# Kernel optimization log

Measured on AMD Instinct MI355X. Metric: run time of the kernel, lower is better.

Reference implementation:

```python
import jax, jax.numpy as jnp
import numpy as np

DIM = 192
HEADS = 4
EPS = 1e-12  # F.normalize default eps


def setup_inputs() -> dict:
    key = jax.random.key(0)
    k0, k1, k2, k3 = jax.random.split(key, 4)
    x = jax.random.normal(k0, (4, DIM, 128, 128), dtype=jnp.float32)
    # qkv 1x1 conv weight: [3*dim, dim, 1, 1] -> stored as [3*dim, dim]
    w_qkv = jax.random.normal(k1, (3 * DIM, DIM), dtype=jnp.float32) * (1.0 / np.sqrt(DIM))
    # depthwise 3x3 conv weight: [3*dim, 1, 3, 3]
    w_dw = jax.random.normal(k2, (3 * DIM, 1, 3, 3), dtype=jnp.float32) * (1.0 / 3.0)
    # project_out 1x1 conv weight: [dim, dim]
    w_proj = jax.random.normal(k3, (DIM, DIM), dtype=jnp.float32) * (1.0 / np.sqrt(DIM))
    # temperature: ones(heads,1,1), requires_grad=False in original
    temperature = jnp.ones((HEADS, 1, 1), dtype=jnp.float32)
    return {"x": x, "w_qkv": w_qkv, "w_dw": w_dw, "w_proj": w_proj,
            "temperature": temperature}


def _l2norm(t):
    # F.normalize(t, dim=-1): t / max(||t||_2, eps)
    n = jnp.sqrt(jnp.sum(t * t, axis=-1, keepdims=True))
    return t / jnp.maximum(n, EPS)


def reference(x, w_qkv, w_dw, w_proj, temperature):
    b, c, h, w = x.shape
    ch = c // HEADS  # channels per head
    # 1x1 conv (no bias) == channel GEMM
    qkv = jnp.einsum('oc,bchw->bohw', w_qkv, x)
    # depthwise 3x3 conv, padding=1, groups=3*dim
    qkv = jax.lax.conv_general_dilated(
        qkv, w_dw, window_strides=(1, 1), padding=((1, 1), (1, 1)),
        dimension_numbers=('NCHW', 'OIHW', 'NCHW'),
        feature_group_count=3 * c)
    q, k, v = jnp.split(qkv, 3, axis=1)
    # b (head ch) h w -> b head ch (h w)
    def rearr(t):
        return t.reshape(b, HEADS, ch, h * w)
    q, k, v = rearr(q), rearr(k), rearr(v)
    q = _l2norm(q)
    k = _l2norm(k)
    # channel-channel attention: [b, head, ch, ch]
    attn = jnp.einsum('bhcn,bhdn->bhcd', q, k) * temperature[None]
    attn = jax.nn.softmax(attn, axis=-1)
    out = jnp.einsum('bhcd,bhdn->bhcn', attn, v)
    out = out.reshape(b, c, h, w)
    out = jnp.einsum('oc,bchw->bohw', w_proj, out)
    return out
```

## Files before the change

### kernel.cpp

```cpp
#include <hip/hip_runtime.h>

typedef unsigned short u16;
typedef float f32x4 __attribute__((ext_vector_type(4)));
typedef __bf16 bf16x8 __attribute__((ext_vector_type(8)));
typedef unsigned short u16x8 __attribute__((ext_vector_type(8)));
typedef unsigned short u16x4 __attribute__((ext_vector_type(4)));

#define DEV static __device__ __forceinline__

DEV u16 f2bf(float f) {
  unsigned int u = __float_as_uint(f);
  u += 0x7FFFu + ((u >> 16) & 1u);
  return (u16)(u >> 16);
}
DEV float bf2f(u16 h) { return __uint_as_float(((unsigned int)h) << 16); }

DEV void gload_lds16(const void* g, void* l) {
  __builtin_amdgcn_global_load_lds(
      (__attribute__((address_space(1))) void*)(unsigned long long)g,
      (__attribute__((address_space(3))) void*)l, 16, 0, 0);
}

__global__ __launch_bounds__(256) void convert_w_kernel(
    const float* __restrict__ in, u16* __restrict__ out, int n) {
  int i = blockIdx.x * 256 + threadIdx.x;
  if (i < n) out[i] = f2bf(in[i]);
}

template <bool IN_F32, bool OUT_BF16, int NJ>
__global__ __launch_bounds__(256, 3) void gemm_bt_kernel(
    const void* __restrict__ Av, const u16* __restrict__ B,
    void* __restrict__ Cv, size_t aBatch, size_t bBatch, size_t cBatch,
    int ldC) {
  __shared__ __align__(16) char smem[49152];
  char* sA = smem;
  char* sB = smem + 24576;

  const int tid = threadIdx.x, wave = tid >> 6, lane = tid & 63;
  const int id = blockIdx.x;
  const int m0 = (id & 255) * 64, b = id >> 8;

  if (IN_F32) {
    const float* Xb = (const float*)Av + (size_t)b * aBatch + m0;
    const int cbl = tid & 15, iq = tid >> 4;
#pragma unroll
    for (int pass = 0; pass < 3; ++pass) {
      const int cb = pass * 16 + cbl;
      f32x4 v[4];
#pragma unroll
      for (int r = 0; r < 4; ++r)
        v[r] = *(const f32x4*)(Xb + (size_t)(cb * 4 + r) * 16384 + iq * 4);
#pragma unroll
      for (int j = 0; j < 4; ++j) {
        const int n = iq * 4 + j;
        u16x4 col;
        col[0] = f2bf(v[0][j]);
        col[1] = f2bf(v[1][j]);
        col[2] = f2bf(v[2][j]);
        col[3] = f2bf(v[3][j]);
        *(u16x4*)(sA + n * 384 + ((cb * 8) ^ ((n & 7) << 4))) = col;
      }
    }
  } else {
    const u16* Vb = (const u16*)Av + (size_t)b * aBatch + m0;
#pragma unroll
    for (int pass = 0; pass < 2; ++pass) {
      const int task = pass * 256 + tid;
      if (task < 384) {
        const int cb = task >> 3, io = task & 7;
        u16x8 v[4];
#pragma unroll
        for (int r = 0; r < 4; ++r)
          v[r] = *(const u16x8*)(Vb + (size_t)(cb * 4 + r) * 16384 + io * 8);
#pragma unroll
        for (int j = 0; j < 8; ++j) {
          const int n = io * 8 + j;
          u16x4 col;
          col[0] = v[0][j];
          col[1] = v[1][j];
          col[2] = v[2][j];
          col[3] = v[3][j];
          *(u16x4*)(sA + n * 384 + ((cb * 8) ^ ((n & 7) << 4))) = col;
        }
      }
    }
  }
  const char* Bbase = (const char*)(B + (size_t)b * bBatch);
#pragma unroll
  for (int i = 0; i < 6; ++i) {
    const int c = i * 4 + wave;
    const int d = c * 1024 + lane * 16;
    const int row = d / 384, inrow = d - row * 384;
    gload_lds16(Bbase + row * 384 + (inrow ^ ((row & 7) << 4)), sB + c * 1024);
  }
  asm volatile("s_waitcnt vmcnt(0) lgkmcnt(0)" ::: "memory");
  __builtin_amdgcn_s_barrier();

  const int wm = wave & 1, wn = wave >> 1;
  const int l15 = lane & 15, lg = lane >> 4;
  const int swm = (l15 & 7) << 4;
  const int rA0 = (wm * 32 + l15) * 384;
  const int rB0 = (wn * 32 + l15) * 384;

  bf16x8 af[2][6];
#pragma unroll
  for (int mi = 0; mi < 2; ++mi)
#pragma unroll
    for (int ks = 0; ks < 6; ++ks)
      af[mi][ks] = *(const bf16x8*)(sA + rA0 + mi * 16 * 384 +
                                    ((ks * 64 + lg * 16) ^ swm));

  f32x4 acc[2][2];
#pragma unroll 1
  for (int j = 0; j < NJ; ++j) {
    bf16x8 bfv[2][6];
#pragma unroll
    for (int nj = 0; nj < 2; ++nj)
#pragma unroll
      for (int ks = 0; ks < 6; ++ks)
        bfv[nj][ks] = *(const bf16x8*)(sB + rB0 + nj * 16 * 384 +
                                       ((ks * 64 + lg * 16) ^ swm));
    asm volatile("s_waitcnt lgkmcnt(0)" ::: "memory");
    __builtin_amdgcn_s_barrier();
    if (j + 1 < NJ) {
      const char* Bj = Bbase + (size_t)(j + 1) * 24576;
#pragma unroll
      for (int i = 0; i < 6; ++i) {
        const int c = i * 4 + wave;
        const int d = c * 1024 + lane * 16;
        const int row = d / 384, inrow = d - row * 384;
        gload_lds16(Bj + row * 384 + (inrow ^ ((row & 7) << 4)), sB + c * 1024);
      }
    }
    if (j > 0) {
      const int j0 = (j - 1) * 64;
      if (OUT_BF16) {
        u16* Cb = (u16*)Cv + (size_t)b * cBatch;
#pragma unroll
        for (int mi = 0; mi < 2; ++mi)
#pragma unroll
          for (int nj = 0; nj < 2; ++nj) {
            u16x4 ov;
#pragma unroll
            for (int r = 0; r < 4; ++r) ov[r] = f2bf(acc[mi][nj][r]);
            *(u16x4*)(Cb + (size_t)(j0 + wn * 32 + nj * 16 + l15) * ldC + m0 +
                      wm * 32 + mi * 16 + lg * 4) = ov;
          }
      } else {
        float* Cb = (float*)Cv + (size_t)b * cBatch;
#pragma unroll
        for (int mi = 0; mi < 2; ++mi)
#pragma unroll
          for (int nj = 0; nj < 2; ++nj)
            *(f32x4*)(Cb + (size_t)(j0 + wn * 32 + nj * 16 + l15) * ldC + m0 +
                      wm * 32 + mi * 16 + lg * 4) = acc[mi][nj];
      }
    }
    __builtin_amdgcn_sched_barrier(0);
#pragma unroll
    for (int mi = 0; mi < 2; ++mi)
#pragma unroll
      for (int nj = 0; nj < 2; ++nj) acc[mi][nj] = (f32x4){0.f, 0.f, 0.f, 0.f};
#pragma unroll
    for (int ks = 0; ks < 6; ++ks)
#pragma unroll
      for (int mi = 0; mi < 2; ++mi)
#pragma unroll
        for (int nj = 0; nj < 2; ++nj)
          acc[mi][nj] = __builtin_amdgcn_mfma_f32_16x16x32_bf16(
              af[mi][ks], bfv[nj][ks], acc[mi][nj], 0, 0, 0);
    if (j + 1 < NJ) {
      if (j == 0)
        asm volatile("s_waitcnt vmcnt(0)" ::: "memory");
      else
        asm volatile("s_waitcnt vmcnt(4)" ::: "memory");
      __builtin_amdgcn_s_barrier();
    }
  }
  {
    const int j0 = (NJ - 1) * 64;
    if (OUT_BF16) {
      u16* Cb = (u16*)Cv + (size_t)b * cBatch;
#pragma unroll
      for (int mi = 0; mi < 2; ++mi)
#pragma unroll
        for (int nj = 0; nj < 2; ++nj) {
          u16x4 ov;
#pragma unroll
          for (int r = 0; r < 4; ++r) ov[r] = f2bf(acc[mi][nj][r]);
          *(u16x4*)(Cb + (size_t)(j0 + wn * 32 + nj * 16 + l15) * ldC + m0 +
                    wm * 32 + mi * 16 + lg * 4) = ov;
        }
    } else {
      float* Cb = (float*)Cv + (size_t)b * cBatch;
#pragma unroll
      for (int mi = 0; mi < 2; ++mi)
#pragma unroll
        for (int nj = 0; nj < 2; ++nj)
          *(f32x4*)(Cb + (size_t)(j0 + wn * 32 + nj * 16 + l15) * ldC + m0 +
                    wm * 32 + mi * 16 + lg * 4) = acc[mi][nj];
    }
  }
}

__global__ __launch_bounds__(256) void dwconv_kernel(
    u16* __restrict__ qkv, const float* __restrict__ wdw,
    float* __restrict__ sq) {
  __shared__ u16 img[16384];
  __shared__ float red[4];
  const int o = blockIdx.x, b = blockIdx.y;
  const size_t base = ((size_t)b * 576 + o) * 16384;
  const int tid = threadIdx.x, wave = tid >> 6, lane = tid & 63;
#pragma unroll
  for (int i = 0; i < 8; ++i) {
    const int off = (i * 4 + wave) * 1024;
    gload_lds16((const char*)qkv + base * 2 + off + lane * 16, (char*)img + off);
  }
  asm volatile("s_waitcnt vmcnt(0)" ::: "memory");
  __syncthreads();
  float w[9];
#pragma unroll
  for (int j = 0; j < 9; ++j) w[j] = wdw[o * 9 + j];
  float sqacc = 0.f;
  for (int it = 0; it < 8; ++it) {
    const int chunk = it * 256 + tid;
    const int px0 = chunk * 8;
    const int y = px0 >> 7, x0 = px0 & 127;
    float acc[8];
#pragma unroll
    for (int j = 0; j < 8; ++j) acc[j] = 0.f;
#pragma unroll
    for (int dy = -1; dy <= 1; ++dy) {
      const int yy = y + dy;
      float v[10];
      if (yy >= 0 && yy <= 127) {
        const u16* rowp = img + yy * 128 + x0;
        u16x8 m = *(const u16x8*)rowp;
#pragma unroll
        for (int j = 0; j < 8; ++j) v[j + 1] = bf2f(m[j]);
        v[0] = (x0 > 0) ? bf2f(rowp[-1]) : 0.f;
        v[9] = (x0 < 120) ? bf2f(rowp[8]) : 0.f;
      } else {
#pragma unroll
        for (int j = 0; j < 10; ++j) v[j] = 0.f;
      }
      const float w0 = w[(dy + 1) * 3], w1 = w[(dy + 1) * 3 + 1],
                  w2 = w[(dy + 1) * 3 + 2];
#pragma unroll
      for (int j = 0; j < 8; ++j) acc[j] += w0 * v[j] + w1 * v[j + 1] + w2 * v[j + 2];
    }
    u16x8 ov;
#pragma unroll
    for (int j = 0; j < 8; ++j) {
      sqacc += acc[j] * acc[j];
      ov[j] = f2bf(acc[j]);
    }
    *(u16x8*)(qkv + base + px0) = ov;
  }
#pragma unroll
  for (int s = 32; s > 0; s >>= 1) sqacc += __shfl_xor(sqacc, s, 64);
  if (lane == 0) red[wave] = sqacc;
  __syncthreads();
  if (tid == 0) sq[b * 576 + o] = red[0] + red[1] + red[2] + red[3];
}

__global__ __launch_bounds__(256) void gram_kernel(
    const u16* __restrict__ qkv, float* __restrict__ partial) {
  __shared__ u16 tiles[4 * 3072];
  __shared__ float red[4 * 2304];
  const int bh = blockIdx.y, b = bh >> 2, h = bh & 3;
  const int g = blockIdx.x;
  const int wave = threadIdx.x >> 6, lane = threadIdx.x & 63;
  const int n0 = g * 512 + wave * 128;
  const u16* qb = qkv + ((size_t)b * 576 + h * 48) * 16384;
  const u16* kb = qb + (size_t)192 * 16384;
  char* tl = (char*)(tiles + wave * 3072);
  const int l15 = lane & 15, lg = lane >> 4;
  const int swz = (l15 & 3) << 4;
  f32x4 acc[3][3];
#pragma unroll
  for (int i = 0; i < 3; ++i)
#pragma unroll
    for (int j = 0; j < 3; ++j) acc[i][j] = (f32x4){0.f, 0.f, 0.f, 0.f};

  for (int ks = 0; ks < 4; ++ks) {
    const int nn = n0 + ks * 32;
    asm volatile("s_waitcnt lgkmcnt(0)" ::: "memory");
#pragma unroll
    for (int i = 0; i < 6; ++i) {
      const int flat = i * 1024 + lane * 16;
      const int row = flat >> 6, colb = flat & 63;
      const u16* src = (row < 48) ? (qb + (size_t)row * 16384 + nn)
                                  : (kb + (size_t)(row - 48) * 16384 + nn);
      gload_lds16((const char*)src + (colb ^ ((row & 3) << 4)), tl + i * 1024);
    }
    asm volatile("s_waitcnt vmcnt(0)" ::: "memory");
    bf16x8 qf[3], kf[3];
#pragma unroll
    for (int f = 0; f < 3; ++f) {
      qf[f] = *(const bf16x8*)(tl + (f * 16 + l15) * 64 + ((lg * 16) ^ swz));
      kf[f] = *(const bf16x8*)(tl + (48 + f * 16 + l15) * 64 + ((lg * 16) ^ swz));
    }
#pragma unroll
    for (int i = 0; i < 3; ++i)
#pragma unroll
      for (int j = 0; j < 3; ++j)
        acc[i][j] = __builtin_amdgcn_mfma_f32_16x16x32_bf16(qf[i], kf[j],
                                                            acc[i][j], 0, 0, 0);
  }
  {
    float* rw = red + wave * 2304;
#pragma unroll
    for (int i = 0; i < 3; ++i)
#pragma unroll
      for (int j = 0; j < 3; ++j)
#pragma unroll
        for (int r = 0; r < 4; ++r)
          rw[(i * 16 + lg * 4 + r) * 48 + (j * 16 + l15)] = acc[i][j][r];
  }
  __syncthreads();
#pragma unroll
  for (int it = 0; it < 9; ++it) {
    const int p = it * 256 + threadIdx.x;
    const float s = red[p] + red[2304 + p] + red[4608 + p] + red[6912 + p];
    partial[((size_t)bh * 2304 + p) * 32 + g] = s;
  }
}

__global__ __launch_bounds__(256) void reduce_partial_kernel(
    const float* __restrict__ partial, float* __restrict__ G) {
  const int idx = blockIdx.x * 256 + threadIdx.x;
  const f32x4* pp = (const f32x4*)(partial + (size_t)idx * 32);
  const f32x4 a = (pp[0] + pp[1]) + (pp[2] + pp[3]) +
                  (pp[4] + pp[5]) + (pp[6] + pp[7]);
  G[idx] = a.x + a.y + a.z + a.w;
}

__global__ __launch_bounds__(256) void softmax_weff_kernel(
    const float* __restrict__ Gin, const float* __restrict__ sq,
    const float* __restrict__ temp, const float* __restrict__ wproj,
    u16* __restrict__ weff) {
  __shared__ float G[2304];
  __shared__ float wp[192 * 49];
  __shared__ float nq[48], nk[48];
  const int bh = blockIdx.x, b = bh >> 2, h = bh & 3;
  const int tid = threadIdx.x;
#pragma unroll
  for (int it = 0; it < 36; ++it) {
    const int j = it * 256 + tid;
    const int o = j / 48, c = j - o * 48;
    wp[o * 49 + c] = wproj[o * 192 + h * 48 + c];
  }
#pragma unroll
  for (int it = 0; it < 9; ++it) {
    const int p = it * 256 + tid;
    G[p] = Gin[(size_t)bh * 2304 + p];
  }
  if (tid < 48) {
    nq[tid] = fmaxf(sqrtf(sq[b * 576 + h * 48 + tid]), 1e-12f);
    nk[tid] = fmaxf(sqrtf(sq[b * 576 + 192 + h * 48 + tid]), 1e-12f);
  }
  __syncthreads();
  if (tid < 48) {
    const int r = tid;
    const float inq = temp[h] / nq[r];
    float L[48];
    float mx = -3.4e38f;
#pragma unroll 4
    for (int d = 0; d < 48; ++d) {
      const float v = G[r * 48 + d] * inq / nk[d];
      L[d] = v;
      mx = fmaxf(mx, v);
    }
    float s = 0.f;
#pragma unroll 4
    for (int d = 0; d < 48; ++d) {
      const float e = __expf(L[d] - mx);
      L[d] = e;
      s += e;
    }
    const float inv = 1.f / s;
#pragma unroll 4
    for (int d = 0; d < 48; ++d) G[r * 48 + d] = L[d] * inv;
  }
  __syncthreads();
  if (tid < 192) {
    const int o = tid;
    f32x4 acc[12];
#pragma unroll
    for (int dv = 0; dv < 12; ++dv) acc[dv] = (f32x4){0.f, 0.f, 0.f, 0.f};
    for (int c = 0; c < 48; ++c) {
      const float w = wp[o * 49 + c];
      const f32x4* at = (const f32x4*)(G + c * 48);
#pragma unroll
      for (int dv = 0; dv < 12; ++dv) acc[dv] += w * at[dv];
    }
    u16* op = weff + ((size_t)b * 192 + o) * 192 + h * 48;
#pragma unroll
    for (int g8 = 0; g8 < 6; ++g8) {
      u16x8 ov;
#pragma unroll
      for (int j = 0; j < 8; ++j) {
        const int d = g8 * 8 + j;
        ov[j] = f2bf(acc[d >> 2][d & 3]);
      }
      *(u16x8*)(op + g8 * 8) = ov;
    }
  }
}

extern "C" void kernel_launch(void* const* d_in, const int* in_sizes, int n_in,
                              void* d_out, int out_size, void* d_ws,
                              size_t ws_size, hipStream_t stream) {
  (void)in_sizes; (void)n_in; (void)out_size; (void)ws_size;
  const float* x      = (const float*)d_in[0];
  const float* w_qkv  = (const float*)d_in[1];
  const float* w_dw   = (const float*)d_in[2];
  const float* w_proj = (const float*)d_in[3];
  const float* temp   = (const float*)d_in[4];

  char* ws = (char*)d_ws;
  u16*   qkv     = (u16*)ws;
  float* partial = (float*)(ws + 75497472);
  float* G       = (float*)(ws + 80216064);
  float* sq      = (float*)(ws + 80363520);
  u16*   Wq      = (u16*)(ws + 80372736);
  u16*   Weff    = (u16*)(ws + 80593920);

  convert_w_kernel<<<dim3(432), 256, 0, stream>>>(w_qkv, Wq, 110592);
  gemm_bt_kernel<true, true, 9><<<dim3(1024), 256, 0, stream>>>(
      x, Wq, qkv, (size_t)192 * 16384, 0, (size_t)576 * 16384, 16384);
  dwconv_kernel<<<dim3(576, 4), 256, 0, stream>>>(qkv, w_dw, sq);
  gram_kernel<<<dim3(32, 16), 256, 0, stream>>>(qkv, partial);
  reduce_partial_kernel<<<dim3(144), 256, 0, stream>>>(partial, G);
  softmax_weff_kernel<<<dim3(16), 256, 0, stream>>>(G, sq, temp, w_proj, Weff);
  gemm_bt_kernel<false, false, 3><<<dim3(1024), 256, 0, stream>>>(
      qkv + (size_t)384 * 16384, Weff, d_out, (size_t)576 * 16384,
      (size_t)192 * 192, (size_t)192 * 16384, 16384);
}
```

Baseline: 131.7 us.

## Double-buffer B tiles in LDS and overlap A-tile load with B prefetch

The GEMM kernel now keeps two B tiles in LDS so each prefetch runs two iterations ahead. The A-tile global loads are issued into registers before the first two B tiles are requested, letting those loads overlap. The loop is fully unrolled so the vmcnt wait thresholds can be compile-time constants. LDS per block grows from 48KB to 72KB and launch bounds drop to 2 blocks per CU, which lowers occupancy. The register-held A prefetch also raises register pressure.

```diff
diff --git a/kernel.cpp b/kernel.cpp
--- a/kernel.cpp
+++ b/kernel.cpp
@@ -21,6 +21,17 @@
       (__attribute__((address_space(3))) void*)l, 16, 0, 0);
 }
 
+DEV void vm_wait(int n) {
+  switch (n) {
+    case 0:  asm volatile("s_waitcnt vmcnt(0)" ::: "memory"); break;
+    case 4:  asm volatile("s_waitcnt vmcnt(4)" ::: "memory"); break;
+    case 6:  asm volatile("s_waitcnt vmcnt(6)" ::: "memory"); break;
+    case 8:  asm volatile("s_waitcnt vmcnt(8)" ::: "memory"); break;
+    case 10: asm volatile("s_waitcnt vmcnt(10)" ::: "memory"); break;
+    default: asm volatile("s_waitcnt vmcnt(14)" ::: "memory"); break;
+  }
+}
+
 __global__ __launch_bounds__(256) void convert_w_kernel(
     const float* __restrict__ in, u16* __restrict__ out, int n) {
   int i = blockIdx.x * 256 + threadIdx.x;
@@ -28,72 +39,94 @@
 }
 
 template <bool IN_F32, bool OUT_BF16, int NJ>
-__global__ __launch_bounds__(256, 3) void gemm_bt_kernel(
+__global__ __launch_bounds__(256, 2) void gemm_bt_kernel(
     const void* __restrict__ Av, const u16* __restrict__ B,
     void* __restrict__ Cv, size_t aBatch, size_t bBatch, size_t cBatch,
     int ldC) {
-  __shared__ __align__(16) char smem[49152];
+  __shared__ __align__(16) char smem[73728];
   char* sA = smem;
-  char* sB = smem + 24576;
 
   const int tid = threadIdx.x, wave = tid >> 6, lane = tid & 63;
   const int id = blockIdx.x;
   const int m0 = (id & 255) * 64, b = id >> 8;
-
+  const char* Bbase = (const char*)(B + (size_t)b * bBatch);
+
+  f32x4 vaf[3][4];
+  u16x8 vau[2][4];
   if (IN_F32) {
     const float* Xb = (const float*)Av + (size_t)b * aBatch + m0;
     const int cbl = tid & 15, iq = tid >> 4;
 #pragma unroll
-    for (int pass = 0; pass < 3; ++pass) {
-      const int cb = pass * 16 + cbl;
-      f32x4 v[4];
+    for (int p = 0; p < 3; ++p)
 #pragma unroll
       for (int r = 0; r < 4; ++r)
-        v[r] = *(const f32x4*)(Xb + (size_t)(cb * 4 + r) * 16384 + iq * 4);
+        vaf[p][r] = *(const f32x4*)(Xb + (size_t)((p * 16 + cbl) * 4 + r) *
+                                             16384 + iq * 4);
+  } else {
+    const u16* Vb = (const u16*)Av + (size_t)b * aBatch + m0;
+#pragma unroll
+    for (int p = 0; p < 2; ++p) {
+      const int task = p * 256 + tid;
+      if (task < 384) {
+        const int cb = task >> 3, io = task & 7;
+#pragma unroll
+        for (int r = 0; r < 4; ++r)
+          vau[p][r] = *(const u16x8*)(Vb + (size_t)(cb * 4 + r) * 16384 +
+                                      io * 8);
+      }
+    }
+  }
+#pragma unroll
+  for (int t = 0; t < 2; ++t) {
+    if (t < NJ) {
+      const char* Bj = Bbase + (size_t)t * 24576;
+      char* sB = smem + 24576 + t * 24576;
+#pragma unroll
+      for (int i = 0; i < 6; ++i) {
+        const int c = i * 4 + wave;
+        const int d = c * 1024 + lane * 16;
+        const int row = d / 384, inrow = d - row * 384;
+        gload_lds16(Bj + row * 384 + (inrow ^ ((row & 7) << 4)), sB + c * 1024);
+      }
+    }
+  }
+  if (IN_F32) {
+    const int cbl = tid & 15, iq = tid >> 4;
+#pragma unroll
+    for (int p = 0; p < 3; ++p) {
+      const int cb = p * 16 + cbl;
 #pragma unroll
       for (int j = 0; j < 4; ++j) {
         const int n = iq * 4 + j;
         u16x4 col;
-        col[0] = f2bf(v[0][j]);
-        col[1] = f2bf(v[1][j]);
-        col[2] = f2bf(v[2][j]);
-        col[3] = f2bf(v[3][j]);
+        col[0] = f2bf(vaf[p][0][j]);
+        col[1] = f2bf(vaf[p][1][j]);
+        col[2] = f2bf(vaf[p][2][j]);
+        col[3] = f2bf(vaf[p][3][j]);
         *(u16x4*)(sA + n * 384 + ((cb * 8) ^ ((n & 7) << 4))) = col;
       }
     }
   } else {
-    const u16* Vb = (const u16*)Av + (size_t)b * aBatch + m0;
-#pragma unroll
-    for (int pass = 0; pass < 2; ++pass) {
-      const int task = pass * 256 + tid;
+#pragma unroll
+    for (int p = 0; p < 2; ++p) {
+      const int task = p * 256 + tid;
       if (task < 384) {
         const int cb = task >> 3, io = task & 7;
-        u16x8 v[4];
-#pragma unroll
-        for (int r = 0; r < 4; ++r)
-          v[r] = *(const u16x8*)(Vb + (size_t)(cb * 4 + r) * 16384 + io * 8);
 #pragma unroll
         for (int j = 0; j < 8; ++j) {
           const int n = io * 8 + j;
           u16x4 col;
-          col[0] = v[0][j];
-          col[1] = v[1][j];
-          col[2] = v[2][j];
-          col[3] = v[3][j];
+          col[0] = vau[p][0][j];
+          col[1] = vau[p][1][j];
+          col[2] = vau[p][2][j];
+          col[3] = vau[p][3][j];
           *(u16x4*)(sA + n * 384 + ((cb * 8) ^ ((n & 7) << 4))) = col;
         }
       }
     }
   }
-  const char* Bbase = (const char*)(B + (size_t)b * bBatch);
-#pragma unroll
-  for (int i = 0; i < 6; ++i) {
-    const int c = i * 4 + wave;
-    const int d = c * 1024 + lane * 16;
-    const int row = d / 384, inrow = d - row * 384;
-    gload_lds16(Bbase + row * 384 + (inrow ^ ((row & 7) << 4)), sB + c * 1024);
-  }
-  asm volatile("s_waitcnt vmcnt(0) lgkmcnt(0)" ::: "memory");
+  asm volatile("s_waitcnt lgkmcnt(0)" ::: "memory");
+  vm_wait(6);
   __builtin_amdgcn_s_barrier();
 
   const int wm = wave & 1, wn = wave >> 1;
@@ -111,8 +144,9 @@
                                     ((ks * 64 + lg * 16) ^ swm));
 
   f32x4 acc[2][2];
-#pragma unroll 1
+#pragma unroll
   for (int j = 0; j < NJ; ++j) {
+    char* sB = smem + 24576 + ((j & 1) ? 24576 : 0);
     bf16x8 bfv[2][6];
 #pragma unroll
     for (int nj = 0; nj < 2; ++nj)
@@ -122,8 +156,8 @@
                                        ((ks * 64 + lg * 16) ^ swm));
     asm volatile("s_waitcnt lgkmcnt(0)" ::: "memory");
     __builtin_amdgcn_s_barrier();
-    if (j + 1 < NJ) {
-      const char* Bj = Bbase + (size_t)(j + 1) * 24576;
+    if (j + 2 < NJ) {
+      const char* Bj = Bbase + (size_t)(j + 2) * 24576;
 #pragma unroll
       for (int i = 0; i < 6; ++i) {
         const int c = i * 4 + wave;
@@ -170,10 +204,7 @@
           acc[mi][nj] = __builtin_amdgcn_mfma_f32_16x16x32_bf16(
               af[mi][ks], bfv[nj][ks], acc[mi][nj], 0, 0, 0);
     if (j + 1 < NJ) {
-      if (j == 0)
-        asm volatile("s_waitcnt vmcnt(0)" ::: "memory");
-      else
-        asm volatile("s_waitcnt vmcnt(4)" ::: "memory");
+      vm_wait((j >= 2 ? 4 : 0) + (j + 3 < NJ ? 6 : 0) + (j >= 1 ? 4 : 0));
       __builtin_amdgcn_s_barrier();
     }
   }
```

Result: slower. 135.1 us (+2.6%).

## Stage GEMM output tiles through LDS for coalesced stores; fold partial reduce into softmax

Applied to the files above, without the earlier changes.

GEMM epilogue now writes each wave's accumulator tile into a per-wave LDS region (reusing the A buffer after a barrier) and reads it back so global stores are full contiguous 16-byte row segments instead of scattered 8/16-byte fragments. The vmcnt wait is adjusted to account for the extra store instructions, and the j loop is fully unrolled. The separate reduce_partial kernel is removed and its 32-way partial sum is done inside softmax_weff, saving a launch and the G round trip. Adds LDS traffic and waits in the epilogue, and the softmax kernel with only 16 blocks now reads all partials itself.

```diff
diff --git a/kernel.cpp b/kernel.cpp
--- a/kernel.cpp
+++ b/kernel.cpp
@@ -19,6 +19,15 @@
   __builtin_amdgcn_global_load_lds(
       (__attribute__((address_space(1))) void*)(unsigned long long)g,
       (__attribute__((address_space(3))) void*)l, 16, 0, 0);
+}
+
+DEV void vm_wait(int n) {
+  switch (n) {
+    case 0:  asm volatile("s_waitcnt vmcnt(0)" ::: "memory"); break;
+    case 2:  asm volatile("s_waitcnt vmcnt(2)" ::: "memory"); break;
+    case 4:  asm volatile("s_waitcnt vmcnt(4)" ::: "memory"); break;
+    default: asm volatile("s_waitcnt vmcnt(6)" ::: "memory"); break;
+  }
 }
 
 __global__ __launch_bounds__(256) void convert_w_kernel(
@@ -39,6 +48,8 @@
   const int tid = threadIdx.x, wave = tid >> 6, lane = tid & 63;
   const int id = blockIdx.x;
   const int m0 = (id & 255) * 64, b = id >> 8;
+  const char* Bbase = (const char*)(B + (size_t)b * bBatch);
+  constexpr int S = OUT_BF16 ? 2 : 4;
 
   if (IN_F32) {
     const float* Xb = (const float*)Av + (size_t)b * aBatch + m0;
@@ -85,7 +96,6 @@
       }
     }
   }
-  const char* Bbase = (const char*)(B + (size_t)b * bBatch);
 #pragma unroll
   for (int i = 0; i < 6; ++i) {
     const int c = i * 4 + wave;
@@ -109,9 +119,55 @@
     for (int ks = 0; ks < 6; ++ks)
       af[mi][ks] = *(const bf16x8*)(sA + rA0 + mi * 16 * 384 +
                                     ((ks * 64 + lg * 16) ^ swm));
+  asm volatile("s_waitcnt lgkmcnt(0)" ::: "memory");
+  __builtin_amdgcn_s_barrier();
+
+  char* rbuf = sA + wave * 6144;
+
+  auto store_tile = [&](int j, const f32x4 acc[2][2]) {
+    const int j0 = j * 64;
+    if (OUT_BF16) {
+#pragma unroll
+      for (int mi = 0; mi < 2; ++mi)
+#pragma unroll
+        for (int nj = 0; nj < 2; ++nj) {
+          u16x4 ov;
+#pragma unroll
+          for (int r = 0; r < 4; ++r) ov[r] = f2bf(acc[mi][nj][r]);
+          *(u16x4*)(rbuf + (nj * 16 + l15) * 72 + mi * 32 + lg * 8) = ov;
+        }
+      asm volatile("s_waitcnt lgkmcnt(0)" ::: "memory");
+      u16* Cb = (u16*)Cv + (size_t)b * cBatch;
+#pragma unroll
+      for (int q = 0; q < 2; ++q) {
+        const int flat = q * 64 + lane;
+        const int row = flat >> 2;
+        const u16x8 val = *(const u16x8*)(rbuf + row * 72 + (flat & 3) * 16);
+        *(u16x8*)(Cb + (size_t)(j0 + wn * 32 + row) * ldC + m0 + wm * 32 +
+                  (flat & 3) * 8) = val;
+      }
+    } else {
+#pragma unroll
+      for (int mi = 0; mi < 2; ++mi)
+#pragma unroll
+        for (int nj = 0; nj < 2; ++nj)
+          *(f32x4*)(rbuf + (nj * 16 + l15) * 144 + mi * 64 + lg * 16) =
+              acc[mi][nj];
+      asm volatile("s_waitcnt lgkmcnt(0)" ::: "memory");
+      float* Cb = (float*)Cv + (size_t)b * cBatch;
+#pragma unroll
+      for (int q = 0; q < 4; ++q) {
+        const int flat = q * 64 + lane;
+        const int row = flat >> 3;
+        const f32x4 val = *(const f32x4*)(rbuf + row * 144 + (flat & 7) * 16);
+        *(f32x4*)(Cb + (size_t)(j0 + wn * 32 + row) * ldC + m0 + wm * 32 +
+                  (flat & 7) * 4) = val;
+      }
+    }
+  };
 
   f32x4 acc[2][2];
-#pragma unroll 1
+#pragma unroll
   for (int j = 0; j < NJ; ++j) {
     bf16x8 bfv[2][6];
 #pragma unroll
@@ -132,30 +188,7 @@
         gload_lds16(Bj + row * 384 + (inrow ^ ((row & 7) << 4)), sB + c * 1024);
       }
     }
-    if (j > 0) {
-      const int j0 = (j - 1) * 64;
-      if (OUT_BF16) {
-        u16* Cb = (u16*)Cv + (size_t)b * cBatch;
-#pragma unroll
-        for (int mi = 0; mi < 2; ++mi)
-#pragma unroll
-          for (int nj = 0; nj < 2; ++nj) {
-            u16x4 ov;
-#pragma unroll
-            for (int r = 0; r < 4; ++r) ov[r] = f2bf(acc[mi][nj][r]);
-            *(u16x4*)(Cb + (size_t)(j0 + wn * 32 + nj * 16 + l15) * ldC + m0 +
-                      wm * 32 + mi * 16 + lg * 4) = ov;
-          }
-      } else {
-        float* Cb = (float*)Cv + (size_t)b * cBatch;
-#pragma unroll
-        for (int mi = 0; mi < 2; ++mi)
-#pragma unroll
-          for (int nj = 0; nj < 2; ++nj)
-            *(f32x4*)(Cb + (size_t)(j0 + wn * 32 + nj * 16 + l15) * ldC + m0 +
-                      wm * 32 + mi * 16 + lg * 4) = acc[mi][nj];
-      }
-    }
+    if (j > 0) store_tile(j - 1, acc);
     __builtin_amdgcn_sched_barrier(0);
 #pragma unroll
     for (int mi = 0; mi < 2; ++mi)
@@ -170,37 +203,11 @@
           acc[mi][nj] = __builtin_amdgcn_mfma_f32_16x16x32_bf16(
               af[mi][ks], bfv[nj][ks], acc[mi][nj], 0, 0, 0);
     if (j + 1 < NJ) {
-      if (j == 0)
-        asm volatile("s_waitcnt vmcnt(0)" ::: "memory");
-      else
-        asm volatile("s_waitcnt vmcnt(4)" ::: "memory");
+      vm_wait(j == 0 ? 0 : S);
       __builtin_amdgcn_s_barrier();
     }
   }
-  {
-    const int j0 = (NJ - 1) * 64;
-    if (OUT_BF16) {
-      u16* Cb = (u16*)Cv + (size_t)b * cBatch;
-#pragma unroll
-      for (int mi = 0; mi < 2; ++mi)
-#pragma unroll
-        for (int nj = 0; nj < 2; ++nj) {
-          u16x4 ov;
-#pragma unroll
-          for (int r = 0; r < 4; ++r) ov[r] = f2bf(acc[mi][nj][r]);
-          *(u16x4*)(Cb + (size_t)(j0 + wn * 32 + nj * 16 + l15) * ldC + m0 +
-                    wm * 32 + mi * 16 + lg * 4) = ov;
-        }
-    } else {
-      float* Cb = (float*)Cv + (size_t)b * cBatch;
-#pragma unroll
-      for (int mi = 0; mi < 2; ++mi)
-#pragma unroll
-        for (int nj = 0; nj < 2; ++nj)
-          *(f32x4*)(Cb + (size_t)(j0 + wn * 32 + nj * 16 + l15) * ldC + m0 +
-                    wm * 32 + mi * 16 + lg * 4) = acc[mi][nj];
-    }
-  }
+  store_tile(NJ - 1, acc);
 }
 
 __global__ __launch_bounds__(256) void dwconv_kernel(
@@ -327,17 +334,8 @@
   }
 }
 
-__global__ __launch_bounds__(256) void reduce_partial_kernel(
-    const float* __restrict__ partial, float* __restrict__ G) {
-  const int idx = blockIdx.x * 256 + threadIdx.x;
-  const f32x4* pp = (const f32x4*)(partial + (size_t)idx * 32);
-  const f32x4 a = (pp[0] + pp[1]) + (pp[2] + pp[3]) +
-                  (pp[4] + pp[5]) + (pp[6] + pp[7]);
-  G[idx] = a.x + a.y + a.z + a.w;
-}
-
 __global__ __launch_bounds__(256) void softmax_weff_kernel(
-    const float* __restrict__ Gin, const float* __restrict__ sq,
+    const float* __restrict__ partial, const float* __restrict__ sq,
     const float* __restrict__ temp, const float* __restrict__ wproj,
     u16* __restrict__ weff) {
   __shared__ float G[2304];
@@ -354,7 +352,10 @@
 #pragma unroll
   for (int it = 0; it < 9; ++it) {
     const int p = it * 256 + tid;
-    G[p] = Gin[(size_t)bh * 2304 + p];
+    const f32x4* pp = (const f32x4*)(partial + ((size_t)bh * 2304 + p) * 32);
+    const f32x4 a = (pp[0] + pp[1]) + (pp[2] + pp[3]) +
+                    (pp[4] + pp[5]) + (pp[6] + pp[7]);
+    G[p] = a.x + a.y + a.z + a.w;
   }
   if (tid < 48) {
     nq[tid] = fmaxf(sqrtf(sq[b * 576 + h * 48 + tid]), 1e-12f);
@@ -422,18 +423,17 @@
   char* ws = (char*)d_ws;
   u16*   qkv     = (u16*)ws;
   float* partial = (float*)(ws + 75497472);
-  float* G       = (float*)(ws + 80216064);
-  float* sq      = (float*)(ws + 80363520);
-  u16*   Wq      = (u16*)(ws + 80372736);
-  u16*   Weff    = (u16*)(ws + 80593920);
+  float* sq      = (float*)(ws + 80216064);
+  u16*   Wq      = (u16*)(ws + 80225280);
+  u16*   Weff    = (u16*)(ws + 80446464);
 
   convert_w_kernel<<<dim3(432), 256, 0, stream>>>(w_qkv, Wq, 110592);
   gemm_bt_kernel<true, true, 9><<<dim3(1024), 256, 0, stream>>>(
       x, Wq, qkv, (size_t)192 * 16384, 0, (size_t)576 * 16384, 16384);
   dwconv_kernel<<<dim3(576, 4), 256, 0, stream>>>(qkv, w_dw, sq);
   gram_kernel<<<dim3(32, 16), 256, 0, stream>>>(qkv, partial);
-  reduce_partial_kernel<<<dim3(144), 256, 0, stream>>>(partial, G);
-  softmax_weff_kernel<<<dim3(16), 256, 0, stream>>>(G, sq, temp, w_proj, Weff);
+  softmax_weff_kernel<<<dim3(16), 256, 0, stream>>>(partial, sq, temp, w_proj,
+                                                    Weff);
   gemm_bt_kernel<false, false, 3><<<dim3(1024), 256, 0, stream>>>(
       qkv + (size_t)384 * 16384, Weff, d_out, (size_t)576 * 16384,
       (size_t)192 * 192, (size_t)192 * 16384, 16384);
```

Result: slower. 136.8 us (+3.9%).
